# Kernel optimization log

Measured on AMD Instinct MI355X. Metric: run time of the kernel, lower is better.

## Reference

```python
import jax, jax.numpy as jnp
import numpy as np

T, B = 512, 64
DIM_INPUT, DIM_LATENT, VOCAB = 512, 1024, 50257


def setup_inputs() -> dict:
    key = jax.random.key(0)
    ks = jax.random.split(key, 12)
    s = 0.02
    return {
        "X": jax.random.randint(ks[0], (T, B), 0, VOCAB, dtype=jnp.int32),
        "h": jax.random.normal(ks[1], (B, DIM_LATENT), dtype=jnp.float32),
        "emb": jax.random.normal(ks[2], (VOCAB, DIM_INPUT), dtype=jnp.float32) * s,
        "Wf": jax.random.normal(ks[3], (DIM_LATENT + DIM_INPUT, DIM_LATENT), dtype=jnp.float32) * s,
        "bf": jnp.zeros((DIM_LATENT,), dtype=jnp.float32),
        "Wi": jax.random.normal(ks[4], (DIM_LATENT + DIM_INPUT, DIM_LATENT), dtype=jnp.float32) * s,
        "bi": jnp.zeros((DIM_LATENT,), dtype=jnp.float32),
        "Wc": jax.random.normal(ks[5], (DIM_LATENT + DIM_INPUT, DIM_LATENT), dtype=jnp.float32) * s,
        "bc": jnp.zeros((DIM_LATENT,), dtype=jnp.float32),
        "Wo": jax.random.normal(ks[6], (DIM_LATENT + DIM_INPUT, DIM_LATENT), dtype=jnp.float32) * s,
        "bo": jnp.zeros((DIM_LATENT,), dtype=jnp.float32),
    }


def reference(X, h, emb, Wf, bf, Wi, bi, Wc, bc, Wo, bo):
    # X: [T, B] int tokens; h: [B, dim_latent]
    xe = emb[X]  # [T, B, dim_input] embedding gather
    c0 = jnp.zeros_like(h)

    def step(carry, x_t):
        h_prev, c_prev = carry
        m = jnp.concatenate([h_prev, x_t], axis=1)  # [B, dl+di]
        ft = jax.nn.sigmoid(m @ Wf + bf)
        it = jax.nn.sigmoid(m @ Wi + bi)
        ct = ft * c_prev + it * jnp.tanh(m @ Wc + bc)
        ot = jax.nn.sigmoid(m @ Wo + bo)
        ht = ot * jnp.tanh(ct)
        return (ht, ct), ht

    (_, _), H = jax.lax.scan(step, (h, c0), xe)
    return H  # [T, B, dim_latent]
```

## Files before the change

### kernel.cpp

```cpp
#include <hip/hip_runtime.h>


namespace {
constexpr int T_STEPS = 512;
constexpr int BATCH   = 64;
constexpr int DI      = 512;
constexpr int DL      = 1024;
constexpr int NKC     = 48;
constexpr int NKC_H   = 32;
constexpr int NBLK    = 256;
constexpr int NTHR    = 320;
constexpr int FPAD    = 32;
constexpr int EPOCH_IDX = NBLK * FPAD;
}

typedef __attribute__((ext_vector_type(8))) short bf16x8;
typedef __attribute__((ext_vector_type(8))) unsigned short u16x8;
typedef __attribute__((ext_vector_type(4))) float f32x4;
typedef __attribute__((ext_vector_type(4))) unsigned int u32x4;
typedef __attribute__((ext_vector_type(2))) unsigned int u32x2;

__device__ __forceinline__ unsigned short f2bf(float x){
  unsigned int u = __float_as_uint(x);
  return (unsigned short)((u + 0x7FFFu + ((u >> 16) & 1u)) >> 16);
}
__device__ __forceinline__ float bf2f(unsigned short b){
  return __uint_as_float(((unsigned int)b) << 16);
}
__device__ __forceinline__ float fast_sigmoid(float v){
  return __fdividef(1.f, 1.f + __expf(-v));
}
__device__ __forceinline__ float fast_tanh(float v){
  v = fminf(fmaxf(v, -15.f), 15.f);
  float t = __expf(2.f * v);
  return __fdividef(t - 1.f, t + 1.f);
}

__global__ void prep_xe(const int* __restrict__ X, const float* __restrict__ emb,
                        unsigned short* __restrict__ xe){
  int i = blockIdx.x * blockDim.x + threadIdx.x;
  const int total = T_STEPS * BATCH * DI / 8;
  if (i >= total) return;
  int row = i >> 6;
  int seg = i & 63;
  int tok = X[row];
  const float* src = emb + (long long)tok * DI + seg * 8;
  float4 v0 = *(const float4*)src;
  float4 v1 = *(const float4*)(src + 4);
  u16x8 o;
  o[0]=f2bf(v0.x); o[1]=f2bf(v0.y); o[2]=f2bf(v0.z); o[3]=f2bf(v0.w);
  o[4]=f2bf(v1.x); o[5]=f2bf(v1.y); o[6]=f2bf(v1.z); o[7]=f2bf(v1.w);
  *(u16x8*)(xe + (long long)row * DI + seg * 8) = o;
}

__global__ void prep_w(const float* __restrict__ Wf, const float* __restrict__ Wi,
                       const float* __restrict__ Wc, const float* __restrict__ Wo,
                       unsigned short* __restrict__ W_hi, unsigned short* __restrict__ W_lo){
  int idx = blockIdx.x * blockDim.x + threadIdx.x;
  if (idx >= 256 * NKC * 64) return;
  int lane = idx & 63;
  int kc   = (idx >> 6) % NKC;
  int bk   = idx / (64 * NKC);
  int lc = lane & 15, kg = lane >> 4;
  int g  = lc >> 2;
  int jl = bk * 4 + (lc & 3);
  const float* Wg = (g == 0) ? Wf : ((g == 1) ? Wi : ((g == 2) ? Wc : Wo));
  int kbase = kc * 32 + kg * 8;
  u16x8 hi, lo;
#pragma unroll
  for (int j = 0; j < 8; j++){
    float wv = Wg[(long long)(kbase + j) * DL + jl];
    unsigned short h = f2bf(wv);
    hi[j] = h;
    lo[j] = f2bf(wv - bf2f(h));
  }
  *(u16x8*)(W_hi + ((long long)(bk * NKC + kc) * 64 + lane) * 8) = hi;
  if (kc < NKC_H)
    *(u16x8*)(W_lo + ((long long)(bk * NKC_H + kc) * 64 + lane) * 8) = lo;
}

__global__ void prep_h(const float* __restrict__ h0,
                       const float* __restrict__ bf_, const float* __restrict__ bi_,
                       const float* __restrict__ bc_, const float* __restrict__ bo_,
                       unsigned short* __restrict__ hB,
                       float* __restrict__ bias_pack, unsigned int* __restrict__ bar){
  int i = blockIdx.x * blockDim.x + threadIdx.x;
  if (i < BATCH * DL) hB[i] = f2bf(h0[i]);
  if (i < 4096){
    int r = i & 3, g = (i >> 2) & 3, bk = i >> 4;
    const float* bg = (g == 0) ? bf_ : ((g == 1) ? bi_ : ((g == 2) ? bc_ : bo_));
    bias_pack[i] = bg[bk * 4 + r];
  }
  if (i < (NBLK + 1) * FPAD) bar[i] = 0u;
}

__launch_bounds__(NTHR, 1)
__global__ void lstm_persist(const unsigned short* __restrict__ xe,
                             const unsigned short* __restrict__ W_hi,
                             const unsigned short* __restrict__ W_lo,
                             unsigned short* __restrict__ hB,
                             const float* __restrict__ bias_pack,
                             float* __restrict__ out,
                             unsigned int* __restrict__ bar){
  extern __shared__ unsigned short lds[];
  unsigned short* lds_hi = lds;
  unsigned short* lds_lo = lds + NKC * 512;
  __shared__ unsigned short stage_h[BATCH * 4];
  __shared__ float          stage_o[BATCH * 4];
  const int tid  = threadIdx.x;
  const int bk   = blockIdx.x;
  const int w    = tid >> 6;
  const int lane = tid & 63;
  const bool isAgg     = (bk == 0) && (w == 4);
  const bool isCompute = (w < 4);

  const uint4* srcHi = (const uint4*)(W_hi + (size_t)bk * NKC * 512);
  uint4* dHi = (uint4*)lds_hi;
  for (int i = tid; i < 3072; i += NTHR) dHi[i] = srcHi[i];
  const uint4* srcLo = (const uint4*)(W_lo + (size_t)bk * NKC_H * 512);
  uint4* dLo = (uint4*)lds_lo;
  for (int i = tid; i < 2048; i += NTHR) dLo[i] = srcLo[i];
  __syncthreads();

  const int lc = lane & 15;
  const int kg = lane >> 4;
  const int g  = lc >> 2;
  const int rowb = (w << 4) + lc;
  const float bias = bias_pack[bk * 16 + lc];
  const int srcBase = (lane & 48) | (lc & 3);
  const int hOff = rowb * DL + kg * 8;
  const int xOff = rowb * DI + kg * 8;
  unsigned int* epochp = bar + EPOCH_IDX;
  float cr0 = 0.f, cr1 = 0.f, cr2 = 0.f, cr3 = 0.f;

  f32x4 acc0 = {0.f,0.f,0.f,0.f}, acc1 = {0.f,0.f,0.f,0.f};
  f32x4 acc2 = {0.f,0.f,0.f,0.f}, acc3 = {0.f,0.f,0.f,0.f};

#define XSTEP(KC, ACC) {                                                        \
    bf16x8 ax = *(const bf16x8*)(xRow + (KC) * 32);                             \
    bf16x8 bh = *(const bf16x8*)(lds_hi + (NKC_H + (KC)) * 512 + lane * 8);     \
    ACC = __builtin_amdgcn_mfma_f32_16x16x32_bf16(ax, bh, ACC, 0, 0, 0); }
#define HSTEP2(KC, ACC) {                                                       \
    bf16x8 ah = *(const bf16x8*)&hv[KC];                                        \
    bf16x8 bh = *(const bf16x8*)(lds_hi + (KC) * 512 + lane * 8);               \
    bf16x8 bl = *(const bf16x8*)(lds_lo + (KC) * 512 + lane * 8);               \
    ACC = __builtin_amdgcn_mfma_f32_16x16x32_bf16(ah, bh, ACC, 0, 0, 0);        \
    ACC = __builtin_amdgcn_mfma_f32_16x16x32_bf16(ah, bl, ACC, 0, 0, 0); }
#define LOADH(I, OFFSTR)                                                        \
    asm volatile("global_load_dwordx4 %0, %1, off offset:" OFFSTR " sc0 sc1"    \
                 : "=v"(hv[I]) : "v"(hbase));

  if (isCompute){
    const unsigned short* xRow = xe + xOff;
#pragma unroll
    for (int kc = 0; kc < 16; kc += 4){
      XSTEP(kc, acc0) XSTEP(kc + 1, acc1) XSTEP(kc + 2, acc2) XSTEP(kc + 3, acc3)
    }
  }

#pragma unroll 1
  for (int t = 0; t < T_STEPS; ++t){
    if (t > 0){
      if (isAgg){
        const unsigned tgt = (unsigned)t;
        int spin = 0;
        for (;;){
          unsigned v0 = __hip_atomic_load(bar + (lane      ) * FPAD, __ATOMIC_RELAXED, __HIP_MEMORY_SCOPE_AGENT);
          unsigned v1 = __hip_atomic_load(bar + (lane +  64) * FPAD, __ATOMIC_RELAXED, __HIP_MEMORY_SCOPE_AGENT);
          unsigned v2 = __hip_atomic_load(bar + (lane + 128) * FPAD, __ATOMIC_RELAXED, __HIP_MEMORY_SCOPE_AGENT);
          unsigned v3 = __hip_atomic_load(bar + (lane + 192) * FPAD, __ATOMIC_RELAXED, __HIP_MEMORY_SCOPE_AGENT);
          bool ok = (v0 >= tgt) & (v1 >= tgt) & (v2 >= tgt) & (v3 >= tgt);
          if (__all(ok ? 1 : 0)) break;
          __builtin_amdgcn_s_sleep(1);
          if (++spin > (1 << 15)) break;
        }
        if (lane == 0)
          __hip_atomic_store(epochp, tgt, __ATOMIC_RELAXED, __HIP_MEMORY_SCOPE_AGENT);
      } else if (w == 0){
        const unsigned tgt = (unsigned)t;
        int spin = 0;
        while (__hip_atomic_load(epochp, __ATOMIC_RELAXED, __HIP_MEMORY_SCOPE_AGENT) < tgt){
          __builtin_amdgcn_s_sleep(1);
          if (++spin > (1 << 16)) break;
        }
      }
    }
    __syncthreads();

    const int rb = t & 1;
    unsigned short* hWr = hB + (rb ^ 1) * (BATCH * DL);
    float* out_t = out + (size_t)t * BATCH * DL;

    if (isCompute){
      u32x4 hv[32];
      const unsigned short* hbase = hB + rb * (BATCH * DL) + hOff;
      LOADH( 0,"0")    LOADH( 1,"64")   LOADH( 2,"128")  LOADH( 3,"192")
      LOADH( 4,"256")  LOADH( 5,"320")  LOADH( 6,"384")  LOADH( 7,"448")
      LOADH( 8,"512")  LOADH( 9,"576")  LOADH(10,"640")  LOADH(11,"704")
      LOADH(12,"768")  LOADH(13,"832")  LOADH(14,"896")  LOADH(15,"960")
      LOADH(16,"1024") LOADH(17,"1088") LOADH(18,"1152") LOADH(19,"1216")
      LOADH(20,"1280") LOADH(21,"1344") LOADH(22,"1408") LOADH(23,"1472")
      LOADH(24,"1536") LOADH(25,"1600") LOADH(26,"1664") LOADH(27,"1728")
      LOADH(28,"1792") LOADH(29,"1856") LOADH(30,"1920") LOADH(31,"1984")
      asm volatile("s_waitcnt vmcnt(0)" ::: "memory");
      __builtin_amdgcn_sched_barrier(0);

#pragma unroll
      for (int kc = 0; kc < NKC_H; kc += 4){
        HSTEP2(kc, acc0) HSTEP2(kc + 1, acc1) HSTEP2(kc + 2, acc2) HSTEP2(kc + 3, acc3)
      }
      f32x4 acc = (acc0 + acc1) + (acc2 + acc3);

      float creg[4] = {cr0, cr1, cr2, cr3};
#pragma unroll
      for (int r = 0; r < 4; r++){
        float v = acc[r] + bias;
        float vF = __shfl(v, srcBase);
        float vI = __shfl(v, srcBase + 4);
        float vC = __shfl(v, srcBase + 8);
        float vO = __shfl(v, srcBase + 12);
        if (g == 0){
          int b = (w << 4) | (kg << 2) | r;
          float ft = fast_sigmoid(vF);
          float it = fast_sigmoid(vI);
          float gt = fast_tanh(vC);
          float ot = fast_sigmoid(vO);
          float cn = ft * creg[r] + it * gt;
          creg[r] = cn;
          float hn = ot * fast_tanh(cn);
          int si = (b << 2) | (lc & 3);
          stage_h[si] = f2bf(hn);
          stage_o[si] = hn;
        }
      }
      cr0 = creg[0]; cr1 = creg[1]; cr2 = creg[2]; cr3 = creg[3];
    }

    __syncthreads();

    if (w == 0){
      u32x2 hv2 = *(const u32x2*)&stage_h[lane << 2];
      u32x4 ov  = *(const u32x4*)&stage_o[lane << 2];
      float4* odst = (float4*)(out_t + lane * DL + (bk << 2));
      *odst = *(const float4*)&ov;
      unsigned short* hdst = hWr + lane * DL + (bk << 2);
      asm volatile("global_store_dwordx2 %0, %1, off sc0 sc1"
                   :: "v"(hdst), "v"(hv2) : "memory");
      asm volatile("s_waitcnt vmcnt(0)" ::: "memory");
      __builtin_amdgcn_sched_barrier(0);
      if (tid == 0)
        __hip_atomic_store(bar + bk * FPAD, (unsigned)(t + 1),
                           __ATOMIC_RELAXED, __HIP_MEMORY_SCOPE_AGENT);
    }

    acc0 = (f32x4){0.f,0.f,0.f,0.f}; acc1 = (f32x4){0.f,0.f,0.f,0.f};
    acc2 = (f32x4){0.f,0.f,0.f,0.f}; acc3 = (f32x4){0.f,0.f,0.f,0.f};
    if (isCompute && t + 1 < T_STEPS){
      const unsigned short* xRow = xe + (size_t)(t + 1) * BATCH * DI + xOff;
#pragma unroll
      for (int kc = 0; kc < 16; kc += 4){
        XSTEP(kc, acc0) XSTEP(kc + 1, acc1) XSTEP(kc + 2, acc2) XSTEP(kc + 3, acc3)
      }
    }
  }
#undef XSTEP
#undef HSTEP2
#undef LOADH
}

extern "C" void kernel_launch(void* const* d_in, const int* in_sizes, int n_in,
                              void* d_out, int out_size, void* d_ws, size_t ws_size,
                              hipStream_t stream){
  const int*   X   = (const int*)d_in[0];
  const float* h0  = (const float*)d_in[1];
  const float* emb = (const float*)d_in[2];
  const float* Wf  = (const float*)d_in[3];
  const float* bf_ = (const float*)d_in[4];
  const float* Wi  = (const float*)d_in[5];
  const float* bi_ = (const float*)d_in[6];
  const float* Wc  = (const float*)d_in[7];
  const float* bc_ = (const float*)d_in[8];
  const float* Wo  = (const float*)d_in[9];
  const float* bo_ = (const float*)d_in[10];
  float* out = (float*)d_out;

  char* ws = (char*)d_ws;
  size_t off = 0;
  auto alloc = [&](size_t bytes) -> void* {
    void* p = ws + off;
    off = (off + bytes + 255) & ~((size_t)255);
    return p;
  };
  unsigned short* xe        = (unsigned short*)alloc(sizeof(unsigned short) * (size_t)T_STEPS * BATCH * DI);
  unsigned short* W_hi      = (unsigned short*)alloc(sizeof(unsigned short) * (size_t)256 * NKC * 512);
  unsigned short* W_lo      = (unsigned short*)alloc(sizeof(unsigned short) * (size_t)256 * NKC_H * 512);
  unsigned short* hB        = (unsigned short*)alloc(sizeof(unsigned short) * 2 * BATCH * DL);
  float*          bias_pack = (float*)alloc(sizeof(float) * 4096);
  unsigned int*   bar       = (unsigned int*)alloc(sizeof(unsigned int) * (NBLK + 1) * FPAD);
  (void)ws_size; (void)in_sizes; (void)n_in; (void)out_size;

  static bool attr_set = false;
  if (!attr_set){
    hipFuncSetAttribute((const void*)lstm_persist,
                        hipFuncAttributeMaxDynamicSharedMemorySize, 160 * 1024);
    attr_set = true;
  }

  hipLaunchKernelGGL(prep_xe, dim3(8192), dim3(256), 0, stream, X, emb, xe);
  hipLaunchKernelGGL(prep_w,  dim3(3072), dim3(256), 0, stream, Wf, Wi, Wc, Wo, W_hi, W_lo);
  hipLaunchKernelGGL(prep_h,  dim3(256),  dim3(256), 0, stream, h0, bf_, bi_, bc_, bo_,
                     hB, bias_pack, bar);
  hipLaunchKernelGGL(lstm_persist, dim3(NBLK), dim3(NTHR), 80 * 1024, stream,
                     xe, W_hi, W_lo, hB, bias_pack, out, bar);
}
```

Baseline: 4.537 ms.

## Replace central epoch barrier with per-block flag polling and split h readiness

Removes the single aggregator block that published a global epoch. Each block now dedicates wave 4 to writing results and polling all peers' flags itself, which takes one global hop out of the per-step dependency chain. Readiness is signalled in two halves, so compute waves can start loading the first half of h before the blocks producing the second half have finished. Block-wide __syncthreads are replaced by LDS counters and fences. The trade-off is far more global polling traffic from 256 blocks, and correctness now rests on subtle workgroup-scope memory ordering.

```diff
diff --git a/kernel.cpp b/kernel.cpp
--- a/kernel.cpp
+++ b/kernel.cpp
@@ -11,7 +11,6 @@
 constexpr int NBLK    = 256;
 constexpr int NTHR    = 320;
 constexpr int FPAD    = 32;
-constexpr int EPOCH_IDX = NBLK * FPAD;
 }
 
 typedef __attribute__((ext_vector_type(8))) short bf16x8;
@@ -34,6 +33,9 @@
   v = fminf(fmaxf(v, -15.f), 15.f);
   float t = __expf(2.f * v);
   return __fdividef(t - 1.f, t + 1.f);
+}
+__device__ __forceinline__ unsigned agent_ld(const unsigned int* p){
+  return __hip_atomic_load(p, __ATOMIC_RELAXED, __HIP_MEMORY_SCOPE_AGENT);
 }
 
 __global__ void prep_xe(const int* __restrict__ X, const float* __restrict__ emb,
@@ -91,7 +93,7 @@
     const float* bg = (g == 0) ? bf_ : ((g == 1) ? bi_ : ((g == 2) ? bc_ : bo_));
     bias_pack[i] = bg[bk * 4 + r];
   }
-  if (i < (NBLK + 1) * FPAD) bar[i] = 0u;
+  if (i < NBLK * FPAD) bar[i] = 0u;
 }
 
 __launch_bounds__(NTHR, 1)
@@ -107,12 +109,11 @@
   unsigned short* lds_lo = lds + NKC * 512;
   __shared__ unsigned short stage_h[BATCH * 4];
   __shared__ float          stage_o[BATCH * 4];
+  __shared__ unsigned int   ldsA, ldsB, cnt1;
   const int tid  = threadIdx.x;
   const int bk   = blockIdx.x;
   const int w    = tid >> 6;
   const int lane = tid & 63;
-  const bool isAgg     = (bk == 0) && (w == 4);
-  const bool isCompute = (w < 4);
 
   const uint4* srcHi = (const uint4*)(W_hi + (size_t)bk * NKC * 512);
   uint4* dHi = (uint4*)lds_hi;
@@ -120,7 +121,62 @@
   const uint4* srcLo = (const uint4*)(W_lo + (size_t)bk * NKC_H * 512);
   uint4* dLo = (uint4*)lds_lo;
   for (int i = tid; i < 2048; i += NTHR) dLo[i] = srcLo[i];
+  if (tid == 0){ ldsA = 0u; ldsB = 0u; cnt1 = 0u; }
   __syncthreads();
+
+  if (w == 4){
+#pragma unroll 1
+    for (int t = 0; t < T_STEPS; ++t){
+      {
+        const unsigned tgt = 4u * (unsigned)(t + 1);
+        int sp = 0;
+        while (__hip_atomic_load(&cnt1, __ATOMIC_RELAXED, __HIP_MEMORY_SCOPE_WORKGROUP) < tgt){
+          if (++sp > (1 << 20)) break;
+        }
+      }
+      __builtin_amdgcn_fence(__ATOMIC_ACQUIRE, "workgroup");
+      const int rb = t & 1;
+      unsigned short* hWr = hB + (rb ^ 1) * (BATCH * DL);
+      float* out_t = out + (size_t)t * BATCH * DL;
+      u32x2  hv2 = *(const u32x2*)&stage_h[lane << 2];
+      float4 ov  = *(const float4*)&stage_o[lane << 2];
+      *(float4*)(out_t + lane * DL + (bk << 2)) = ov;
+      unsigned short* hdst = hWr + lane * DL + (bk << 2);
+      asm volatile("global_store_dwordx2 %0, %1, off sc0 sc1"
+                   :: "v"(hdst), "v"(hv2) : "memory");
+      asm volatile("s_waitcnt vmcnt(0)" ::: "memory");
+      __builtin_amdgcn_sched_barrier(0);
+      if (lane == 0)
+        __hip_atomic_store(bar + bk * FPAD, (unsigned)(t + 1),
+                           __ATOMIC_RELAXED, __HIP_MEMORY_SCOPE_AGENT);
+      if (t + 1 < T_STEPS){
+        const unsigned tg2 = (unsigned)(t + 1);
+        {
+          int sp = 0;
+          for (;;){
+            unsigned v0 = agent_ld(bar + (lane      ) * FPAD);
+            unsigned v1 = agent_ld(bar + (lane +  64) * FPAD);
+            if (__all(((v0 >= tg2) & (v1 >= tg2)) ? 1 : 0)) break;
+            __builtin_amdgcn_s_sleep(1);
+            if (++sp > (1 << 15)) break;
+          }
+          __hip_atomic_store(&ldsA, tg2, __ATOMIC_RELAXED, __HIP_MEMORY_SCOPE_WORKGROUP);
+        }
+        {
+          int sp = 0;
+          for (;;){
+            unsigned v2 = agent_ld(bar + (lane + 128) * FPAD);
+            unsigned v3 = agent_ld(bar + (lane + 192) * FPAD);
+            if (__all(((v2 >= tg2) & (v3 >= tg2)) ? 1 : 0)) break;
+            __builtin_amdgcn_s_sleep(1);
+            if (++sp > (1 << 15)) break;
+          }
+          __hip_atomic_store(&ldsB, tg2, __ATOMIC_RELAXED, __HIP_MEMORY_SCOPE_WORKGROUP);
+        }
+      }
+    }
+    return;
+  }
 
   const int lc = lane & 15;
   const int kg = lane >> 4;
@@ -130,7 +186,6 @@
   const int srcBase = (lane & 48) | (lc & 3);
   const int hOff = rowb * DL + kg * 8;
   const int xOff = rowb * DI + kg * 8;
-  unsigned int* epochp = bar + EPOCH_IDX;
   float cr0 = 0.f, cr1 = 0.f, cr2 = 0.f, cr3 = 0.f;
 
   f32x4 acc0 = {0.f,0.f,0.f,0.f}, acc1 = {0.f,0.f,0.f,0.f};
@@ -150,7 +205,7 @@
     asm volatile("global_load_dwordx4 %0, %1, off offset:" OFFSTR " sc0 sc1"    \
                  : "=v"(hv[I]) : "v"(hbase));
 
-  if (isCompute){
+  {
     const unsigned short* xRow = xe + xOff;
 #pragma unroll
     for (int kc = 0; kc < 16; kc += 4){
@@ -160,102 +215,70 @@
 
 #pragma unroll 1
   for (int t = 0; t < T_STEPS; ++t){
+    const int rb = t & 1;
+    u32x4 hv[32];
+    const unsigned short* hbase = hB + rb * (BATCH * DL) + hOff;
+
     if (t > 0){
-      if (isAgg){
-        const unsigned tgt = (unsigned)t;
-        int spin = 0;
-        for (;;){
-          unsigned v0 = __hip_atomic_load(bar + (lane      ) * FPAD, __ATOMIC_RELAXED, __HIP_MEMORY_SCOPE_AGENT);
-          unsigned v1 = __hip_atomic_load(bar + (lane +  64) * FPAD, __ATOMIC_RELAXED, __HIP_MEMORY_SCOPE_AGENT);
-          unsigned v2 = __hip_atomic_load(bar + (lane + 128) * FPAD, __ATOMIC_RELAXED, __HIP_MEMORY_SCOPE_AGENT);
-          unsigned v3 = __hip_atomic_load(bar + (lane + 192) * FPAD, __ATOMIC_RELAXED, __HIP_MEMORY_SCOPE_AGENT);
-          bool ok = (v0 >= tgt) & (v1 >= tgt) & (v2 >= tgt) & (v3 >= tgt);
-          if (__all(ok ? 1 : 0)) break;
-          __builtin_amdgcn_s_sleep(1);
-          if (++spin > (1 << 15)) break;
-        }
-        if (lane == 0)
-          __hip_atomic_store(epochp, tgt, __ATOMIC_RELAXED, __HIP_MEMORY_SCOPE_AGENT);
-      } else if (w == 0){
-        const unsigned tgt = (unsigned)t;
-        int spin = 0;
-        while (__hip_atomic_load(epochp, __ATOMIC_RELAXED, __HIP_MEMORY_SCOPE_AGENT) < tgt){
-          __builtin_amdgcn_s_sleep(1);
-          if (++spin > (1 << 16)) break;
-        }
-      }
-    }
-    __syncthreads();
-
-    const int rb = t & 1;
-    unsigned short* hWr = hB + (rb ^ 1) * (BATCH * DL);
-    float* out_t = out + (size_t)t * BATCH * DL;
-
-    if (isCompute){
-      u32x4 hv[32];
-      const unsigned short* hbase = hB + rb * (BATCH * DL) + hOff;
-      LOADH( 0,"0")    LOADH( 1,"64")   LOADH( 2,"128")  LOADH( 3,"192")
-      LOADH( 4,"256")  LOADH( 5,"320")  LOADH( 6,"384")  LOADH( 7,"448")
-      LOADH( 8,"512")  LOADH( 9,"576")  LOADH(10,"640")  LOADH(11,"704")
-      LOADH(12,"768")  LOADH(13,"832")  LOADH(14,"896")  LOADH(15,"960")
-      LOADH(16,"1024") LOADH(17,"1088") LOADH(18,"1152") LOADH(19,"1216")
-      LOADH(20,"1280") LOADH(21,"1344") LOADH(22,"1408") LOADH(23,"1472")
-      LOADH(24,"1536") LOADH(25,"1600") LOADH(26,"1664") LOADH(27,"1728")
-      LOADH(28,"1792") LOADH(29,"1856") LOADH(30,"1920") LOADH(31,"1984")
-      asm volatile("s_waitcnt vmcnt(0)" ::: "memory");
-      __builtin_amdgcn_sched_barrier(0);
-
-#pragma unroll
-      for (int kc = 0; kc < NKC_H; kc += 4){
-        HSTEP2(kc, acc0) HSTEP2(kc + 1, acc1) HSTEP2(kc + 2, acc2) HSTEP2(kc + 3, acc3)
-      }
-      f32x4 acc = (acc0 + acc1) + (acc2 + acc3);
-
-      float creg[4] = {cr0, cr1, cr2, cr3};
-#pragma unroll
-      for (int r = 0; r < 4; r++){
-        float v = acc[r] + bias;
-        float vF = __shfl(v, srcBase);
-        float vI = __shfl(v, srcBase + 4);
-        float vC = __shfl(v, srcBase + 8);
-        float vO = __shfl(v, srcBase + 12);
-        if (g == 0){
-          int b = (w << 4) | (kg << 2) | r;
-          float ft = fast_sigmoid(vF);
-          float it = fast_sigmoid(vI);
-          float gt = fast_tanh(vC);
-          float ot = fast_sigmoid(vO);
-          float cn = ft * creg[r] + it * gt;
-          creg[r] = cn;
-          float hn = ot * fast_tanh(cn);
-          int si = (b << 2) | (lc & 3);
-          stage_h[si] = f2bf(hn);
-          stage_o[si] = hn;
-        }
-      }
-      cr0 = creg[0]; cr1 = creg[1]; cr2 = creg[2]; cr3 = creg[3];
-    }
-
-    __syncthreads();
-
-    if (w == 0){
-      u32x2 hv2 = *(const u32x2*)&stage_h[lane << 2];
-      u32x4 ov  = *(const u32x4*)&stage_o[lane << 2];
-      float4* odst = (float4*)(out_t + lane * DL + (bk << 2));
-      *odst = *(const float4*)&ov;
-      unsigned short* hdst = hWr + lane * DL + (bk << 2);
-      asm volatile("global_store_dwordx2 %0, %1, off sc0 sc1"
-                   :: "v"(hdst), "v"(hv2) : "memory");
-      asm volatile("s_waitcnt vmcnt(0)" ::: "memory");
-      __builtin_amdgcn_sched_barrier(0);
-      if (tid == 0)
-        __hip_atomic_store(bar + bk * FPAD, (unsigned)(t + 1),
-                           __ATOMIC_RELAXED, __HIP_MEMORY_SCOPE_AGENT);
-    }
+      int sp = 0;
+      while (__hip_atomic_load(&ldsA, __ATOMIC_RELAXED, __HIP_MEMORY_SCOPE_WORKGROUP) < (unsigned)t){
+        if (++sp > (1 << 20)) break;
+      }
+    }
+    LOADH( 0,"0")    LOADH( 1,"64")   LOADH( 2,"128")  LOADH( 3,"192")
+    LOADH( 4,"256")  LOADH( 5,"320")  LOADH( 6,"384")  LOADH( 7,"448")
+    LOADH( 8,"512")  LOADH( 9,"576")  LOADH(10,"640")  LOADH(11,"704")
+    LOADH(12,"768")  LOADH(13,"832")  LOADH(14,"896")  LOADH(15,"960")
+    if (t > 0){
+      int sp = 0;
+      while (__hip_atomic_load(&ldsB, __ATOMIC_RELAXED, __HIP_MEMORY_SCOPE_WORKGROUP) < (unsigned)t){
+        if (++sp > (1 << 20)) break;
+      }
+    }
+    LOADH(16,"1024") LOADH(17,"1088") LOADH(18,"1152") LOADH(19,"1216")
+    LOADH(20,"1280") LOADH(21,"1344") LOADH(22,"1408") LOADH(23,"1472")
+    LOADH(24,"1536") LOADH(25,"1600") LOADH(26,"1664") LOADH(27,"1728")
+    LOADH(28,"1792") LOADH(29,"1856") LOADH(30,"1920") LOADH(31,"1984")
+    asm volatile("s_waitcnt vmcnt(0)" ::: "memory");
+    __builtin_amdgcn_sched_barrier(0);
+
+#pragma unroll
+    for (int kc = 0; kc < NKC_H; kc += 4){
+      HSTEP2(kc, acc0) HSTEP2(kc + 1, acc1) HSTEP2(kc + 2, acc2) HSTEP2(kc + 3, acc3)
+    }
+    f32x4 acc = (acc0 + acc1) + (acc2 + acc3);
+
+    float creg[4] = {cr0, cr1, cr2, cr3};
+#pragma unroll
+    for (int r = 0; r < 4; r++){
+      float v = acc[r] + bias;
+      float vF = __shfl(v, srcBase);
+      float vI = __shfl(v, srcBase + 4);
+      float vC = __shfl(v, srcBase + 8);
+      float vO = __shfl(v, srcBase + 12);
+      if (g == 0){
+        int b = (w << 4) | (kg << 2) | r;
+        float ft = fast_sigmoid(vF);
+        float it = fast_sigmoid(vI);
+        float gt = fast_tanh(vC);
+        float ot = fast_sigmoid(vO);
+        float cn = ft * creg[r] + it * gt;
+        creg[r] = cn;
+        float hn = ot * fast_tanh(cn);
+        int si = (b << 2) | (lc & 3);
+        stage_h[si] = f2bf(hn);
+        stage_o[si] = hn;
+      }
+    }
+    cr0 = creg[0]; cr1 = creg[1]; cr2 = creg[2]; cr3 = creg[3];
+
+    __builtin_amdgcn_fence(__ATOMIC_RELEASE, "workgroup");
+    if (lane == 0)
+      __hip_atomic_fetch_add(&cnt1, 1u, __ATOMIC_RELAXED, __HIP_MEMORY_SCOPE_WORKGROUP);
 
     acc0 = (f32x4){0.f,0.f,0.f,0.f}; acc1 = (f32x4){0.f,0.f,0.f,0.f};
     acc2 = (f32x4){0.f,0.f,0.f,0.f}; acc3 = (f32x4){0.f,0.f,0.f,0.f};
-    if (isCompute && t + 1 < T_STEPS){
+    if (t + 1 < T_STEPS){
       const unsigned short* xRow = xe + (size_t)(t + 1) * BATCH * DI + xOff;
 #pragma unroll
       for (int kc = 0; kc < 16; kc += 4){
@@ -296,7 +319,7 @@
   unsigned short* W_lo      = (unsigned short*)alloc(sizeof(unsigned short) * (size_t)256 * NKC_H * 512);
   unsigned short* hB        = (unsigned short*)alloc(sizeof(unsigned short) * 2 * BATCH * DL);
   float*          bias_pack = (float*)alloc(sizeof(float) * 4096);
-  unsigned int*   bar       = (unsigned int*)alloc(sizeof(unsigned int) * (NBLK + 1) * FPAD);
+  unsigned int*   bar       = (unsigned int*)alloc(sizeof(unsigned int) * NBLK * FPAD);
   (void)ws_size; (void)in_sizes; (void)n_in; (void)out_size;
 
   static bool attr_set = false;
```

Result: slower. 6.759 ms (+49.0%).

## Read previous hidden state from fp32 output instead of separate bf16 buffer

Applied to the files above, without the earlier changes.

Drops the bf16 double-buffered hidden-state array and has each step read h_{t-1} directly from the fp32 output slice (or h0 at t=0), converting to bf16 in registers with packed convert instructions. Each step now issues one coherent store instead of two and no longer needs the h conversion in prep_h. In exchange, each step reads twice as many bytes from L2/global per recurrence step. The explicit batched asm loads with a single wait are replaced by plain loads the compiler schedules, which may add latency on the critical serial path.

```diff
diff --git a/kernel.cpp b/kernel.cpp
--- a/kernel.cpp
+++ b/kernel.cpp
@@ -18,7 +18,6 @@
 typedef __attribute__((ext_vector_type(8))) unsigned short u16x8;
 typedef __attribute__((ext_vector_type(4))) float f32x4;
 typedef __attribute__((ext_vector_type(4))) unsigned int u32x4;
-typedef __attribute__((ext_vector_type(2))) unsigned int u32x2;
 
 __device__ __forceinline__ unsigned short f2bf(float x){
   unsigned int u = __float_as_uint(x);
@@ -79,13 +78,10 @@
     *(u16x8*)(W_lo + ((long long)(bk * NKC_H + kc) * 64 + lane) * 8) = lo;
 }
 
-__global__ void prep_h(const float* __restrict__ h0,
-                       const float* __restrict__ bf_, const float* __restrict__ bi_,
+__global__ void prep_h(const float* __restrict__ bf_, const float* __restrict__ bi_,
                        const float* __restrict__ bc_, const float* __restrict__ bo_,
-                       unsigned short* __restrict__ hB,
                        float* __restrict__ bias_pack, unsigned int* __restrict__ bar){
   int i = blockIdx.x * blockDim.x + threadIdx.x;
-  if (i < BATCH * DL) hB[i] = f2bf(h0[i]);
   if (i < 4096){
     int r = i & 3, g = (i >> 2) & 3, bk = i >> 4;
     const float* bg = (g == 0) ? bf_ : ((g == 1) ? bi_ : ((g == 2) ? bc_ : bo_));
@@ -98,15 +94,14 @@
 __global__ void lstm_persist(const unsigned short* __restrict__ xe,
                              const unsigned short* __restrict__ W_hi,
                              const unsigned short* __restrict__ W_lo,
-                             unsigned short* __restrict__ hB,
+                             const float* __restrict__ h0,
                              const float* __restrict__ bias_pack,
                              float* __restrict__ out,
                              unsigned int* __restrict__ bar){
   extern __shared__ unsigned short lds[];
   unsigned short* lds_hi = lds;
   unsigned short* lds_lo = lds + NKC * 512;
-  __shared__ unsigned short stage_h[BATCH * 4];
-  __shared__ float          stage_o[BATCH * 4];
+  __shared__ float stage_o[BATCH * 4];
   const int tid  = threadIdx.x;
   const int bk   = blockIdx.x;
   const int w    = tid >> 6;
@@ -141,14 +136,18 @@
     bf16x8 bh = *(const bf16x8*)(lds_hi + (NKC_H + (KC)) * 512 + lane * 8);     \
     ACC = __builtin_amdgcn_mfma_f32_16x16x32_bf16(ax, bh, ACC, 0, 0, 0); }
 #define HSTEP2(KC, ACC) {                                                       \
-    bf16x8 ah = *(const bf16x8*)&hv[KC];                                        \
+    float4 f0 = hRow4[(KC) * 8];                                                \
+    float4 f1 = hRow4[(KC) * 8 + 1];                                            \
+    u32x4 pk;                                                                   \
+    asm("v_cvt_pk_bf16_f32 %0, %1, %2" : "=v"(pk[0]) : "v"(f0.x), "v"(f0.y));   \
+    asm("v_cvt_pk_bf16_f32 %0, %1, %2" : "=v"(pk[1]) : "v"(f0.z), "v"(f0.w));   \
+    asm("v_cvt_pk_bf16_f32 %0, %1, %2" : "=v"(pk[2]) : "v"(f1.x), "v"(f1.y));   \
+    asm("v_cvt_pk_bf16_f32 %0, %1, %2" : "=v"(pk[3]) : "v"(f1.z), "v"(f1.w));   \
+    bf16x8 ah = *(bf16x8*)&pk;                                                  \
     bf16x8 bh = *(const bf16x8*)(lds_hi + (KC) * 512 + lane * 8);               \
     bf16x8 bl = *(const bf16x8*)(lds_lo + (KC) * 512 + lane * 8);               \
     ACC = __builtin_amdgcn_mfma_f32_16x16x32_bf16(ah, bh, ACC, 0, 0, 0);        \
     ACC = __builtin_amdgcn_mfma_f32_16x16x32_bf16(ah, bl, ACC, 0, 0, 0); }
-#define LOADH(I, OFFSTR)                                                        \
-    asm volatile("global_load_dwordx4 %0, %1, off offset:" OFFSTR " sc0 sc1"    \
-                 : "=v"(hv[I]) : "v"(hbase));
 
   if (isCompute){
     const unsigned short* xRow = xe + xOff;
@@ -187,23 +186,11 @@
     }
     __syncthreads();
 
-    const int rb = t & 1;
-    unsigned short* hWr = hB + (rb ^ 1) * (BATCH * DL);
-    float* out_t = out + (size_t)t * BATCH * DL;
+    const float* hsrc = (t == 0) ? h0 : (out + (size_t)(t - 1) * (BATCH * DL));
+    float* out_t = out + (size_t)t * (BATCH * DL);
 
     if (isCompute){
-      u32x4 hv[32];
-      const unsigned short* hbase = hB + rb * (BATCH * DL) + hOff;
-      LOADH( 0,"0")    LOADH( 1,"64")   LOADH( 2,"128")  LOADH( 3,"192")
-      LOADH( 4,"256")  LOADH( 5,"320")  LOADH( 6,"384")  LOADH( 7,"448")
-      LOADH( 8,"512")  LOADH( 9,"576")  LOADH(10,"640")  LOADH(11,"704")
-      LOADH(12,"768")  LOADH(13,"832")  LOADH(14,"896")  LOADH(15,"960")
-      LOADH(16,"1024") LOADH(17,"1088") LOADH(18,"1152") LOADH(19,"1216")
-      LOADH(20,"1280") LOADH(21,"1344") LOADH(22,"1408") LOADH(23,"1472")
-      LOADH(24,"1536") LOADH(25,"1600") LOADH(26,"1664") LOADH(27,"1728")
-      LOADH(28,"1792") LOADH(29,"1856") LOADH(30,"1920") LOADH(31,"1984")
-      asm volatile("s_waitcnt vmcnt(0)" ::: "memory");
-      __builtin_amdgcn_sched_barrier(0);
+      const float4* hRow4 = (const float4*)(hsrc + hOff);
 
 #pragma unroll
       for (int kc = 0; kc < NKC_H; kc += 4){
@@ -228,9 +215,7 @@
           float cn = ft * creg[r] + it * gt;
           creg[r] = cn;
           float hn = ot * fast_tanh(cn);
-          int si = (b << 2) | (lc & 3);
-          stage_h[si] = f2bf(hn);
-          stage_o[si] = hn;
+          stage_o[(b << 2) | (lc & 3)] = hn;
         }
       }
       cr0 = creg[0]; cr1 = creg[1]; cr2 = creg[2]; cr3 = creg[3];
@@ -239,13 +224,10 @@
     __syncthreads();
 
     if (w == 0){
-      u32x2 hv2 = *(const u32x2*)&stage_h[lane << 2];
-      u32x4 ov  = *(const u32x4*)&stage_o[lane << 2];
-      float4* odst = (float4*)(out_t + lane * DL + (bk << 2));
-      *odst = *(const float4*)&ov;
-      unsigned short* hdst = hWr + lane * DL + (bk << 2);
-      asm volatile("global_store_dwordx2 %0, %1, off sc0 sc1"
-                   :: "v"(hdst), "v"(hv2) : "memory");
+      f32x4 ov = *(const f32x4*)&stage_o[lane << 2];
+      float* odst = out_t + lane * DL + (bk << 2);
+      asm volatile("global_store_dwordx4 %0, %1, off sc0 sc1"
+                   :: "v"(odst), "v"(ov) : "memory");
       asm volatile("s_waitcnt vmcnt(0)" ::: "memory");
       __builtin_amdgcn_sched_barrier(0);
       if (tid == 0)
@@ -265,7 +247,6 @@
   }
 #undef XSTEP
 #undef HSTEP2
-#undef LOADH
 }
 
 extern "C" void kernel_launch(void* const* d_in, const int* in_sizes, int n_in,
@@ -294,7 +275,6 @@
   unsigned short* xe        = (unsigned short*)alloc(sizeof(unsigned short) * (size_t)T_STEPS * BATCH * DI);
   unsigned short* W_hi      = (unsigned short*)alloc(sizeof(unsigned short) * (size_t)256 * NKC * 512);
   unsigned short* W_lo      = (unsigned short*)alloc(sizeof(unsigned short) * (size_t)256 * NKC_H * 512);
-  unsigned short* hB        = (unsigned short*)alloc(sizeof(unsigned short) * 2 * BATCH * DL);
   float*          bias_pack = (float*)alloc(sizeof(float) * 4096);
   unsigned int*   bar       = (unsigned int*)alloc(sizeof(unsigned int) * (NBLK + 1) * FPAD);
   (void)ws_size; (void)in_sizes; (void)n_in; (void)out_size;
@@ -308,8 +288,8 @@
 
   hipLaunchKernelGGL(prep_xe, dim3(8192), dim3(256), 0, stream, X, emb, xe);
   hipLaunchKernelGGL(prep_w,  dim3(3072), dim3(256), 0, stream, Wf, Wi, Wc, Wo, W_hi, W_lo);
-  hipLaunchKernelGGL(prep_h,  dim3(256),  dim3(256), 0, stream, h0, bf_, bi_, bc_, bo_,
-                     hB, bias_pack, bar);
+  hipLaunchKernelGGL(prep_h,  dim3(256),  dim3(256), 0, stream, bf_, bi_, bc_, bo_,
+                     bias_pack, bar);
   hipLaunchKernelGGL(lstm_persist, dim3(NBLK), dim3(NTHR), 80 * 1024, stream,
-                     xe, W_hi, W_lo, hB, bias_pack, out, bar);
-}
+                     xe, W_hi, W_lo, h0, bias_pack, out, bar);
+}
```

After: 5.572 ms. 1.23x slower.
